# Kernel optimization log

Hardware: AMD Instinct MI355X
Metric: run time of the kernel (lower is better)

The kernel has to match this reference:

```python
import jax, jax.numpy as jnp
import numpy as np
import math

D_MODEL = 1024
N_HEADS = 16
D_K = D_MODEL // N_HEADS
B, S = 4, 1024
MAX_REL = 64  # table built for 2*64-1 positions, clamped beyond


def setup_inputs() -> dict:
    key = jax.random.key(0)
    ks = jax.random.split(key, 11)
    init = 1.0 / math.sqrt(D_MODEL)
    def lin(k):
        kw, kb = jax.random.split(k)
        W = jax.random.uniform(kw, (D_MODEL, D_MODEL), jnp.float32, -init, init)
        b = jax.random.uniform(kb, (D_MODEL,), jnp.float32, -init, init)
        return W, b
    wq, bq = lin(ks[0]); wk, bk = lin(ks[1]); wv, bv = lin(ks[2]); wo, bo = lin(ks[3])
    x = jax.random.normal(ks[4], (B, S, D_MODEL), jnp.float32)
    rel_table = jax.random.normal(ks[5], (2 * MAX_REL - 1, N_HEADS), jnp.float32)
    mask = jnp.ones((B, 1, 1, S), jnp.int32)
    return {"x": x, "mask": mask, "wq": wq, "bq": bq, "wk": wk, "bk": bk,
            "wv": wv, "bv": bv, "wo": wo, "bo": bo, "rel_table": rel_table}


def reference(x, mask, wq, bq, wk, bk, wv, bv, wo, bo, rel_table):
    Bn, Sn, Dm = x.shape
    scale = math.sqrt(D_K)
    def heads(y):  # [B,S,D] -> [B,H,S,dk]
        return y.reshape(Bn, Sn, N_HEADS, D_K).transpose(0, 2, 1, 3)
    Q = heads(x @ wq.T + bq)
    K = heads(x @ wk.T + bk)
    V = heads(x @ wv.T + bv)
    scores = jnp.einsum('bhqd,bhkd->bhqk', Q, K) / scale
    # relative position bias gather, clamped to table range
    rel = jnp.arange(Sn)[None, :] - jnp.arange(Sn)[:, None] + MAX_REL - 1
    rel = jnp.clip(rel, 0, 2 * MAX_REL - 2)
    bias = rel_table[rel]                      # [S,S,H]
    scores = scores + bias.transpose(2, 0, 1)[None]  # [B,H,S,S]
    scores = jnp.where(mask == 0, jnp.float32(-1e9), scores)
    attn = jax.nn.softmax(scores, axis=-1)
    ctx = jnp.einsum('bhqk,bhkd->bhqd', attn, V)
    ctx = ctx.transpose(0, 2, 1, 3).reshape(Bn, Sn, Dm)
    return ctx @ wo.T + bo
```

## Files before the change

### kernel.cpp

```cpp
#include <hip/hip_runtime.h>
#include <hip/hip_bf16.h>

typedef __attribute__((ext_vector_type(8))) short short8;
typedef __attribute__((ext_vector_type(4))) short short4v;
typedef __attribute__((ext_vector_type(4))) float f32x4;

#define D_MODEL 1024
#define N_HEADS 16
#define D_KK 64
#define BATCH 4
#define SEQ 1024
#define NTOK (BATCH*SEQ)

#define LOG2E  1.44269504f
#define SCALE2 (0.125f * 1.44269504f)
#define NEGBIG (-1.44269504e9f)

#if __has_builtin(__builtin_amdgcn_mfma_f32_16x16x16bf16_1k)
#define HAVE_MFMA16 1
#else
#define HAVE_MFMA16 0
#endif

#if __has_builtin(__builtin_amdgcn_exp2f)
#define EXP2(x) __builtin_amdgcn_exp2f(x)
#else
#define EXP2(x) exp2f(x)
#endif

template<int N> struct ic { static constexpr int value = N; };

__device__ __forceinline__ short f2b(float f){
  unsigned u = __float_as_uint(f);
  u += 0x7fffu + ((u >> 16) & 1u);
  return (short)(u >> 16);
}

__device__ __forceinline__ void gl2lds16(const void* g, void* l){
  __builtin_amdgcn_global_load_lds(
      (const __attribute__((address_space(1))) void*)g,
      (__attribute__((address_space(3))) void*)l, 16, 0, 0);
}

__device__ __forceinline__ float max3f(float a, float b, float c){
  float d; asm("v_max3_f32 %0, %1, %2, %3" : "=v"(d) : "v"(a), "v"(b), "v"(c)); return d;
}
__device__ __forceinline__ float tmax16(const f32x4* sc){
  float t = max3f(sc[0][0], sc[0][1], sc[0][2]);
  t = max3f(t, sc[0][3], sc[1][0]);
  t = max3f(t, sc[1][1], sc[1][2]);
  t = max3f(t, sc[1][3], sc[2][0]);
  t = max3f(t, sc[2][1], sc[2][2]);
  t = max3f(t, sc[2][3], sc[3][0]);
  t = max3f(t, sc[3][1], sc[3][2]);
  return fmaxf(t, sc[3][3]);
}

__global__ __launch_bounds__(256) void cvt_all_kernel(
    const float* __restrict__ x,  const float* __restrict__ wq,
    const float* __restrict__ wk, const float* __restrict__ wv,
    const float* __restrict__ wo, short* __restrict__ dst)
{
  const size_t NX = (size_t)NTOK * D_MODEL;
  const size_t NW = (size_t)D_MODEL * D_MODEL;
  size_t e = ((size_t)blockIdx.x * 256 + threadIdx.x) * 4;
  const float* s;
  size_t off;
  if      (e < NX)        { s = x;  off = e; }
  else if (e < NX +   NW) { s = wq; off = e - NX; }
  else if (e < NX + 2*NW) { s = wk; off = e - NX -   NW; }
  else if (e < NX + 3*NW) { s = wv; off = e - NX - 2*NW; }
  else                    { s = wo; off = e - NX - 3*NW; }
  f32x4 v = *reinterpret_cast<const f32x4*>(s + off);
  short4v o;
  o[0]=f2b(v[0]); o[1]=f2b(v[1]); o[2]=f2b(v[2]); o[3]=f2b(v[3]);
  *reinterpret_cast<short4v*>(dst + e) = o;
}

__global__ __launch_bounds__(256) void qkv_gemm_kernel(
    const short* __restrict__ X,
    const short* __restrict__ Wq, const short* __restrict__ Wk, const short* __restrict__ Wv,
    const float* __restrict__ bq, const float* __restrict__ bk, const float* __restrict__ bv,
    short* __restrict__ Q, short* __restrict__ K, short* __restrict__ V)
{
  __shared__ short As[128*64];
  __shared__ short Bs[3][64*64];
  const int bid = blockIdx.x;
  const int xcd = bid & 7, s = bid >> 3;
  const int bn0 = (s >> 2) * 64;
  const int bm0 = (xcd * 4 + (s & 3)) * 128;

  const int tid = threadIdx.x, lane = tid & 63, w = tid >> 6;
  const int wr = w >> 1, wc = w & 1;
  const int srow = lane >> 3;
  const int scol = ((lane & 7) ^ srow) * 8;
  const int fr = lane & 15, g = lane >> 4;

  const short* const Wz[3] = {Wq, Wk, Wv};

  f32x4 acc[3][4][2];
  #pragma unroll
  for (int z=0;z<3;z++)
    #pragma unroll
    for (int m=0;m<4;m++)
      #pragma unroll
      for (int n=0;n<2;n++) acc[z][m][n] = (f32x4){0.f,0.f,0.f,0.f};

  for (int k0 = 0; k0 < D_MODEL; k0 += 64){
    __syncthreads();
    #pragma unroll
    for (int i=0;i<4;i++){
      const int c = w*4 + i;
      gl2lds16(X + (size_t)(bm0 + c*8 + srow)*D_MODEL + k0 + scol, &As[c*8*64]);
    }
    #pragma unroll
    for (int z=0;z<3;z++)
      #pragma unroll
      for (int i=0;i<2;i++){
        const int c = w*2 + i;
        gl2lds16(Wz[z] + (size_t)(bn0 + c*8 + srow)*D_MODEL + k0 + scol, &Bs[z][c*8*64]);
      }
    __syncthreads();
    #pragma unroll
    for (int f=0; f<2; f++){
      short8 af[4];
      #pragma unroll
      for (int m=0;m<4;m++){
        const int rr = wr*64 + m*16 + fr;
        af[m] = *reinterpret_cast<const short8*>(
            (const char*)As + rr*128 + ((g*16 + f*64) ^ ((rr&7)<<4)));
      }
      #pragma unroll
      for (int z=0;z<3;z++){
        short8 bfr[2];
        #pragma unroll
        for (int n=0;n<2;n++){
          const int rr = wc*32 + n*16 + fr;
          bfr[n] = *reinterpret_cast<const short8*>(
              (const char*)&Bs[z][0] + rr*128 + ((g*16 + f*64) ^ ((rr&7)<<4)));
        }
        #pragma unroll
        for (int m=0;m<4;m++)
          #pragma unroll
          for (int n=0;n<2;n++)
            acc[z][m][n] = __builtin_amdgcn_mfma_f32_16x16x32_bf16(af[m], bfr[n], acc[z][m][n], 0,0,0);
      }
    }
  }

  #pragma unroll
  for (int z=0;z<3;z++){
    const float* bias = (z==0) ? bq : (z==1) ? bk : bv;
    #pragma unroll
    for (int n=0;n<2;n++){
      const int col = bn0 + wc*32 + n*16 + fr;
      const float bv_ = bias[col];
      #pragma unroll
      for (int m=0;m<4;m++){
        const int row0 = bm0 + wr*64 + m*16 + g*4;
        if (z == 2){
          const int hh = col >> 6, dd = col & 63;
          const int bb = row0 >> 10, ss = row0 & 1023;
          short4v o;
          #pragma unroll
          for (int r=0;r<4;r++) o[r] = f2b(acc[z][m][n][r] + bv_);
          *reinterpret_cast<short4v*>(
              V + ((size_t)(bb*N_HEADS+hh)*D_KK + dd)*SEQ + ss) = o;
        } else {
          short* O = (z==0) ? Q : K;
          #pragma unroll
          for (int r=0;r<4;r++){
            float v = acc[z][m][n][r] + bv_;
            if (z == 0) v *= SCALE2;
            O[(size_t)(row0+r)*D_MODEL + col] = f2b(v);
          }
        }
      }
    }
  }
}

template<int BN, int MODE, bool PRESC>
__device__ __forceinline__ void gemm_bt_body(const short* __restrict__ A,
    const short* __restrict__ W, const float* __restrict__ bias,
    void* __restrict__ Cout, int N, int K, int bm0, int bn0,
    short* AsB, short* BsB)
{
  constexpr int NF = BN / 32;
  const int tid = threadIdx.x, lane = tid & 63, w = tid >> 6;
  const int wr = w >> 1, wc = w & 1;
  const int srow = lane >> 3;
  const int scol = ((lane & 7) ^ srow) * 8;
  const int fr = lane & 15, g = lane >> 4;

  f32x4 acc[4][NF];
  #pragma unroll
  for (int m=0;m<4;m++)
    #pragma unroll
    for (int n=0;n<NF;n++) acc[m][n] = (f32x4){0.f,0.f,0.f,0.f};

  for (int k0 = 0; k0 < K; k0 += 64){
    __syncthreads();
    #pragma unroll
    for (int i=0;i<4;i++){
      const int c = w*4 + i;
      gl2lds16(A + (size_t)(bm0 + c*8 + srow)*K + k0 + scol, &AsB[c*8*64]);
    }
    #pragma unroll
    for (int i=0;i<NF;i++){
      const int c = w*NF + i;
      gl2lds16(W + (size_t)(bn0 + c*8 + srow)*K + k0 + scol, &BsB[c*8*64]);
    }
    __syncthreads();
    #pragma unroll
    for (int f=0; f<2; f++){
      short8 af[4], bfr[NF];
      #pragma unroll
      for (int m=0;m<4;m++){
        const int rr = wr*64 + m*16 + fr;
        af[m] = *reinterpret_cast<const short8*>(
            (const char*)AsB + rr*128 + ((g*16 + f*64) ^ ((rr&7)<<4)));
      }
      #pragma unroll
      for (int n=0;n<NF;n++){
        const int rr = wc*(BN/2) + n*16 + fr;
        bfr[n] = *reinterpret_cast<const short8*>(
            (const char*)BsB + rr*128 + ((g*16 + f*64) ^ ((rr&7)<<4)));
      }
      #pragma unroll
      for (int m=0;m<4;m++)
        #pragma unroll
        for (int n=0;n<NF;n++)
          acc[m][n] = __builtin_amdgcn_mfma_f32_16x16x32_bf16(af[m], bfr[n], acc[m][n], 0,0,0);
    }
  }

  #pragma unroll
  for (int n=0;n<NF;n++){
    const int col = bn0 + wc*(BN/2) + n*16 + fr;
    const float bv = bias[col];
    #pragma unroll
    for (int m=0;m<4;m++){
      const int row0 = bm0 + wr*64 + m*16 + g*4;
      #pragma unroll
      for (int r=0;r<4;r++){
        float v = acc[m][n][r] + bv;
        if (PRESC) v *= SCALE2;
        if (MODE == 1) ((float*)Cout)[(size_t)(row0+r)*N + col] = v;
        else           ((short*)Cout)[(size_t)(row0+r)*N + col] = f2b(v);
      }
    }
  }
}

__global__ __launch_bounds__(256) void out_gemm_kernel(
    const short* __restrict__ Ctx, const short* __restrict__ Wo,
    const float* __restrict__ bo, float* __restrict__ Out)
{
  __shared__ short As[128*64];
  __shared__ short Bs[64*64];
  const int bid = blockIdx.x;
  const int xcd = bid & 7, s = bid >> 3;
  const int bn0 = (s >> 2) * 64;
  const int bm0 = (xcd * 4 + (s & 3)) * 128;
  gemm_bt_body<64,1,false>(Ctx, Wo, bo, Out, D_MODEL, D_MODEL, bm0, bn0, As, Bs);
}

__global__ __launch_bounds__(512, 2) void attn_kernel(
    const short* __restrict__ Qb, const short* __restrict__ Kb,
    const short* __restrict__ Vtg, const int* __restrict__ mask,
    const float* __restrict__ rel_table, short* __restrict__ Ctx)
{
  const int bid = blockIdx.x;
  const int xcd = bid & 7, slot = bid >> 3;
  const int bh = xcd * 8 + (slot >> 3);
  const int qt = slot & 7;
  const int b = bh >> 4, h = bh & 15;
  const int q0 = qt * 128;
  const int tid = threadIdx.x, lane = tid & 63, w = tid >> 6;
  const int team = w >> 2, wt = w & 3;
  const int fr = lane & 15, g = lane >> 4;

  __shared__ short kvbuf[2][2][2][64][64];
  __shared__ float rel_pad[384];
  __shared__ float mb_all[2][8][64];
  __shared__ float ml[128][2];

  for (int i = tid; i < 384; i += 512){
    int d = i - 128;
    d = d < 0 ? 0 : (d > 126 ? 126 : d);
    rel_pad[i] = rel_table[d * N_HEADS + h] * LOG2E;
  }
  const float cb_lo = rel_table[0*N_HEADS + h]   * LOG2E;
  const float cb_hi = rel_table[126*N_HEADS + h] * LOG2E;

  for (int e = tid; e < 1024; e += 512){
    const int tm = e >> 9, tt = (e >> 6) & 7, i = e & 63;
    const int kvt = tm*512 + tt*64;
    const int delta = kvt - q0;
    const bool far = (delta <= -128 || delta >= 192);
    const float cb = far ? (delta > 0 ? cb_hi : cb_lo) : 0.f;
    mb_all[tm][tt][i] = mask[b*SEQ + kvt + i] ? cb : NEGBIG;
  }

  const short* Qg = Qb + (size_t)b*SEQ*D_MODEL + h*D_KK;
  const short* Kg = Kb + (size_t)b*SEQ*D_MODEL + h*D_KK;
  const short* Vg = Vtg + (size_t)bh*D_KK*SEQ;

  const int qa = q0 + wt*32 + fr;
  const int qb = qa + 16;
  short8 qfa[2], qfb[2];
  #pragma unroll
  for (int f=0; f<2; f++){
    qfa[f] = *reinterpret_cast<const short8*>(Qg + (size_t)qa*D_MODEL + g*8 + f*32);
    qfb[f] = *reinterpret_cast<const short8*>(Qg + (size_t)qb*D_MODEL + g*8 + f*32);
  }

  const char* lds0 = (const char*)kvbuf;
  const int swzb = (fr & 7) << 4;
  const char* kp[2];
  #pragma unroll
  for (int f=0; f<2; f++)
    kp[f] = lds0 + team*16384 + fr*128 + ((g*16 + f*64) ^ swzb);
  const char* vp[4];
  #pragma unroll
  for (int kt=0; kt<4; kt++)
    vp[kt] = lds0 + 32768 + team*16384 + fr*128
           + ((((kt*2 + (g>>1)) ^ (fr&7)) << 4) + (g&1)*8);
  const char* mbp0 = (const char*)mb_all + team*2048 + g*16;

  f32x4 ctxa[4], ctxb[4];
  #pragma unroll
  for (int dt=0; dt<4; dt++){ ctxa[dt] = (f32x4){0.f,0.f,0.f,0.f}; ctxb[dt] = ctxa[dt]; }
  float mruna = -3.0e38f, lruna = 0.f, mrunb = -3.0e38f, lrunb = 0.f;

  const int srow = lane >> 3;
  const int scol = ((lane & 7) ^ srow) * 8;
  auto stage = [&](int buf, int kv0){
    #pragma unroll
    for (int i=0;i<2;i++){
      const int c = wt*2 + i;
      gl2lds16(Kg + (size_t)(kv0 + c*8 + srow)*D_MODEL + scol, &kvbuf[0][team][buf][c*8][0]);
      gl2lds16(Vg + (size_t)(c*8 + srow)*SEQ + kv0 + scol,     &kvbuf[1][team][buf][c*8][0]);
    }
  };

  auto tile_step = [&](auto BUFC, auto VMC, int kv0, int tt) __attribute__((always_inline)) {
    constexpr int BUFL = decltype(BUFC)::value;
    constexpr int VM   = decltype(VMC)::value;

    if constexpr (VM == 4) asm volatile("s_waitcnt vmcnt(4)" ::: "memory");
    else                   asm volatile("s_waitcnt vmcnt(0)" ::: "memory");
    __builtin_amdgcn_s_barrier();
    asm volatile("" ::: "memory");

    const char* mbp = mbp0 + tt*256;

    f32x4 sca[4], scb[4];
    const int delta = kv0 - q0;
    if (delta <= -128 || delta >= 192){
      #pragma unroll
      for (int kt=0;kt<4;kt++){
        f32x4 mb4 = *reinterpret_cast<const f32x4*>(mbp + kt*64);
        sca[kt] = mb4;
        scb[kt] = mb4;
      }
    } else {
      const int pbase = delta + 63 - (wt*32 + fr) + 128 + g*4;
      f32x4 rr[5];
      #pragma unroll
      for (int j=0;j<5;j++)
        #pragma unroll
        for (int r=0;r<4;r++)
          rr[j][r] = rel_pad[pbase - 16 + j*16 + r];
      #pragma unroll
      for (int kt=0;kt<4;kt++){
        f32x4 mb4 = *reinterpret_cast<const f32x4*>(mbp + kt*64);
        #pragma unroll
        for (int r=0;r<4;r++){
          sca[kt][r] = rr[kt+1][r] + mb4[r];
          scb[kt][r] = rr[kt][r]   + mb4[r];
        }
      }
    }

    __builtin_amdgcn_s_setprio(1);
    #pragma unroll
    for (int kt=0;kt<4;kt++){
      #pragma unroll
      for (int f=0;f<2;f++){
        short8 kf = *reinterpret_cast<const short8*>(kp[f] + (kt*2048 + BUFL*8192));
        sca[kt] = __builtin_amdgcn_mfma_f32_16x16x32_bf16(kf, qfa[f], sca[kt], 0,0,0);
        scb[kt] = __builtin_amdgcn_mfma_f32_16x16x32_bf16(kf, qfb[f], scb[kt], 0,0,0);
      }
    }
    __builtin_amdgcn_s_setprio(0);

    short4v paa[4], pab[4];
    {
      const float tmax = tmax16(sca);
      if (!__all(tmax <= mruna + 8.f)){
        float tm = fmaxf(tmax, __shfl_xor(tmax, 16));
        tm = fmaxf(tm, __shfl_xor(tm, 32));
        const float mnew = fmaxf(mruna, tm);
        const float corr = EXP2(mruna - mnew);
        lruna *= corr;
        #pragma unroll
        for (int dt=0;dt<4;dt++)
          #pragma unroll
          for (int r=0;r<4;r++) ctxa[dt][r] *= corr;
        mruna = mnew;
      }
      float psum = 0.f;
      #pragma unroll
      for (int kt=0;kt<4;kt++){
        float p0 = EXP2(sca[kt][0] - mruna);
        float p1 = EXP2(sca[kt][1] - mruna);
        float p2 = EXP2(sca[kt][2] - mruna);
        float p3 = EXP2(sca[kt][3] - mruna);
        psum += (p0 + p1) + (p2 + p3);
        union { short4v s; __hip_bfloat162 hh[2]; } u;
        u.hh[0] = __float22bfloat162_rn(make_float2(p0, p1));
        u.hh[1] = __float22bfloat162_rn(make_float2(p2, p3));
        paa[kt] = u.s;
      }
      lruna += psum;
    }
    {
      const float tmax = tmax16(scb);
      if (!__all(tmax <= mrunb + 8.f)){
        float tm = fmaxf(tmax, __shfl_xor(tmax, 16));
        tm = fmaxf(tm, __shfl_xor(tm, 32));
        const float mnew = fmaxf(mrunb, tm);
        const float corr = EXP2(mrunb - mnew);
        lrunb *= corr;
        #pragma unroll
        for (int dt=0;dt<4;dt++)
          #pragma unroll
          for (int r=0;r<4;r++) ctxb[dt][r] *= corr;
        mrunb = mnew;
      }
      float psum = 0.f;
      #pragma unroll
      for (int kt=0;kt<4;kt++){
        float p0 = EXP2(scb[kt][0] - mrunb);
        float p1 = EXP2(scb[kt][1] - mrunb);
        float p2 = EXP2(scb[kt][2] - mrunb);
        float p3 = EXP2(scb[kt][3] - mrunb);
        psum += (p0 + p1) + (p2 + p3);
        union { short4v s; __hip_bfloat162 hh[2]; } u;
        u.hh[0] = __float22bfloat162_rn(make_float2(p0, p1));
        u.hh[1] = __float22bfloat162_rn(make_float2(p2, p3));
        pab[kt] = u.s;
      }
      lrunb += psum;
    }

    __builtin_amdgcn_s_setprio(1);
#if HAVE_MFMA16
    #pragma unroll
    for (int dt=0;dt<4;dt++){
      #pragma unroll
      for (int kt=0;kt<4;kt++){
        short4v va = *reinterpret_cast<const short4v*>(vp[kt] + (dt*2048 + BUFL*8192));
        ctxa[dt] = __builtin_amdgcn_mfma_f32_16x16x16bf16_1k(va, paa[kt], ctxa[dt], 0,0,0);
        ctxb[dt] = __builtin_amdgcn_mfma_f32_16x16x16bf16_1k(va, pab[kt], ctxb[dt], 0,0,0);
      }
    }
#else
    const char* vsb = lds0 + 32768 + team*16384 + BUFL*8192;
    #pragma unroll
    for (int f=0;f<2;f++){
      union { short8 s8; unsigned u[4]; } bfa, bfb;
      #pragma unroll
      for (int m=0;m<4;m++){
        const int srcl = ((g&1)*2 + (m>>1))*16 + fr;
        union { short4v s; unsigned u[2]; } ca0, ca1, cb0, cb1;
        ca0.s = paa[f*2+0]; ca1.s = paa[f*2+1];
        cb0.s = pab[f*2+0]; cb1.s = pab[f*2+1];
        unsigned a0 = __shfl((int)ca0.u[m&1], srcl);
        unsigned a1 = __shfl((int)ca1.u[m&1], srcl);
        bfa.u[m] = (g >> 1) ? a1 : a0;
        unsigned b0 = __shfl((int)cb0.u[m&1], srcl);
        unsigned b1 = __shfl((int)cb1.u[m&1], srcl);
        bfb.u[m] = (g >> 1) ? b1 : b0;
      }
      #pragma unroll
      for (int dt=0;dt<4;dt++){
        const int dr = dt*16 + fr;
        const int vswz = (dr & 7) << 4;
        short8 va = *reinterpret_cast<const short8*>(
            vsb + dr*128 + ((g*16 + f*64) ^ vswz));
        ctxa[dt] = __builtin_amdgcn_mfma_f32_16x16x32_bf16(va, bfa.s8, ctxa[dt], 0,0,0);
        ctxb[dt] = __builtin_amdgcn_mfma_f32_16x16x32_bf16(va, bfb.s8, ctxb[dt], 0,0,0);
      }
    }
#endif
    __builtin_amdgcn_s_setprio(0);

    asm volatile("" ::: "memory");
    __builtin_amdgcn_s_barrier();
  };

  const int kvbase = team * 512;
  __syncthreads();
  stage(0, kvbase);
  stage(1, kvbase + 64);

  for (int t = 0; t < 6; t += 2){
    tile_step(ic<0>{}, ic<4>{}, kvbase + t*64,     t);
    stage(0, kvbase + (t+2)*64);
    tile_step(ic<1>{}, ic<4>{}, kvbase + (t+1)*64, t+1);
    stage(1, kvbase + (t+3)*64);
  }
  tile_step(ic<0>{}, ic<4>{}, kvbase + 6*64, 6);
  tile_step(ic<1>{}, ic<0>{}, kvbase + 7*64, 7);
  asm volatile("" ::: "memory");

  lruna += __shfl_xor(lruna, 16);
  lruna += __shfl_xor(lruna, 32);
  lrunb += __shfl_xor(lrunb, 16);
  lrunb += __shfl_xor(lrunb, 32);

  float* mctx = (float*)&kvbuf[0][0][0][0][0];
  const int rowA = wt*32 + fr, rowB = rowA + 16;
  if (team == 1){
    #pragma unroll
    for (int dt=0;dt<4;dt++){
      *reinterpret_cast<f32x4*>(&mctx[rowA*72 + dt*16 + g*4]) = ctxa[dt];
      *reinterpret_cast<f32x4*>(&mctx[rowB*72 + dt*16 + g*4]) = ctxb[dt];
    }
    ml[rowA][0] = mruna; ml[rowA][1] = lruna;
    ml[rowB][0] = mrunb; ml[rowB][1] = lrunb;
  }
  __syncthreads();
  if (team == 0){
    {
      const float m1 = ml[rowA][0], l1 = ml[rowA][1];
      const float m  = fmaxf(mruna, m1);
      const float s0 = EXP2(mruna - m), s1 = EXP2(m1 - m);
      const float rl = 1.f / (lruna*s0 + l1*s1);
      #pragma unroll
      for (int dt=0;dt<4;dt++){
        f32x4 c1 = *reinterpret_cast<const f32x4*>(&mctx[rowA*72 + dt*16 + g*4]);
        short4v o;
        #pragma unroll
        for (int r=0;r<4;r++) o[r] = f2b((ctxa[dt][r]*s0 + c1[r]*s1) * rl);
        *reinterpret_cast<short4v*>(
            Ctx + (size_t)(b*SEQ + qa)*D_MODEL + h*D_KK + dt*16 + g*4) = o;
      }
    }
    {
      const float m1 = ml[rowB][0], l1 = ml[rowB][1];
      const float m  = fmaxf(mrunb, m1);
      const float s0 = EXP2(mrunb - m), s1 = EXP2(m1 - m);
      const float rl = 1.f / (lrunb*s0 + l1*s1);
      #pragma unroll
      for (int dt=0;dt<4;dt++){
        f32x4 c1 = *reinterpret_cast<const f32x4*>(&mctx[rowB*72 + dt*16 + g*4]);
        short4v o;
        #pragma unroll
        for (int r=0;r<4;r++) o[r] = f2b((ctxb[dt][r]*s0 + c1[r]*s1) * rl);
        *reinterpret_cast<short4v*>(
            Ctx + (size_t)(b*SEQ + qb)*D_MODEL + h*D_KK + dt*16 + g*4) = o;
      }
    }
  }
}

extern "C" void kernel_launch(void* const* d_in, const int* in_sizes, int n_in,
                              void* d_out, int out_size, void* d_ws, size_t ws_size,
                              hipStream_t stream) {
  const float* x    = (const float*)d_in[0];
  const int*   mask = (const int*)  d_in[1];
  const float* wq   = (const float*)d_in[2];
  const float* bq   = (const float*)d_in[3];
  const float* wk   = (const float*)d_in[4];
  const float* bk   = (const float*)d_in[5];
  const float* wv   = (const float*)d_in[6];
  const float* bv   = (const float*)d_in[7];
  const float* wo   = (const float*)d_in[8];
  const float* bo   = (const float*)d_in[9];
  const float* rel  = (const float*)d_in[10];

  const size_t NX = (size_t)NTOK * D_MODEL;
  const size_t NW = (size_t)D_MODEL * D_MODEL;
  if (ws_size < (NX + 4*NW + 4*NX) * sizeof(short)) return;
  short* xb   = (short*)d_ws;
  short* wqb  = xb  + NX;
  short* wkb  = wqb + NW;
  short* wvb  = wkb + NW;
  short* wob  = wvb + NW;
  short* Qb   = wob + NW;
  short* Kb   = Qb  + NX;
  short* Vtg  = Kb  + NX;
  short* Ctxb = Vtg + NX;

  cvt_all_kernel<<<8192, 256, 0, stream>>>(x, wq, wk, wv, wo, xb);

  qkv_gemm_kernel<<<512, 256, 0, stream>>>(
      xb, wqb, wkb, wvb, bq, bk, bv, Qb, Kb, Vtg);

  attn_kernel<<<512, 512, 0, stream>>>(Qb, Kb, Vtg, mask, rel, Ctxb);

  out_gemm_kernel<<<512, 256, 0, stream>>>(Ctxb, wob, bo, (float*)d_out);
}
```

Measured before the change: 100.3 us.

## Double-buffer LDS tiles in QKV GEMM with vmcnt-based async prefetch

```diff
diff --git a/kernel.cpp b/kernel.cpp
--- a/kernel.cpp
+++ b/kernel.cpp
@@ -83,8 +83,8 @@
     const float* __restrict__ bq, const float* __restrict__ bk, const float* __restrict__ bv,
     short* __restrict__ Q, short* __restrict__ K, short* __restrict__ V)
 {
-  __shared__ short As[128*64];
-  __shared__ short Bs[3][64*64];
+  __shared__ short As[2][128*64];
+  __shared__ short Bs[2][3][64*64];
   const int bid = blockIdx.x;
   const int xcd = bid & 7, s = bid >> 3;
   const int bn0 = (s >> 2) * 64;
@@ -106,21 +106,29 @@
       #pragma unroll
       for (int n=0;n<2;n++) acc[z][m][n] = (f32x4){0.f,0.f,0.f,0.f};
 
-  for (int k0 = 0; k0 < D_MODEL; k0 += 64){
-    __syncthreads();
+  auto stage = [&](int buf, int t){
+    const int k0 = t * 64;
     #pragma unroll
     for (int i=0;i<4;i++){
       const int c = w*4 + i;
-      gl2lds16(X + (size_t)(bm0 + c*8 + srow)*D_MODEL + k0 + scol, &As[c*8*64]);
+      gl2lds16(X + (size_t)(bm0 + c*8 + srow)*D_MODEL + k0 + scol, &As[buf][c*8*64]);
     }
     #pragma unroll
     for (int z=0;z<3;z++)
       #pragma unroll
       for (int i=0;i<2;i++){
         const int c = w*2 + i;
-        gl2lds16(Wz[z] + (size_t)(bn0 + c*8 + srow)*D_MODEL + k0 + scol, &Bs[z][c*8*64]);
-      }
-    __syncthreads();
+        gl2lds16(Wz[z] + (size_t)(bn0 + c*8 + srow)*D_MODEL + k0 + scol, &Bs[buf][z][c*8*64]);
+      }
+  };
+
+  auto kstep = [&](auto BUFC, auto VMC) __attribute__((always_inline)) {
+    constexpr int BUFL = decltype(BUFC)::value;
+    constexpr int VM   = decltype(VMC)::value;
+    if constexpr (VM == 10) asm volatile("s_waitcnt vmcnt(10)" ::: "memory");
+    else                    asm volatile("s_waitcnt vmcnt(0)"  ::: "memory");
+    __builtin_amdgcn_s_barrier();
+    asm volatile("" ::: "memory");
     #pragma unroll
     for (int f=0; f<2; f++){
       short8 af[4];
@@ -128,7 +136,7 @@
       for (int m=0;m<4;m++){
         const int rr = wr*64 + m*16 + fr;
         af[m] = *reinterpret_cast<const short8*>(
-            (const char*)As + rr*128 + ((g*16 + f*64) ^ ((rr&7)<<4)));
+            (const char*)&As[BUFL][0] + rr*128 + ((g*16 + f*64) ^ ((rr&7)<<4)));
       }
       #pragma unroll
       for (int z=0;z<3;z++){
@@ -137,7 +145,7 @@
         for (int n=0;n<2;n++){
           const int rr = wc*32 + n*16 + fr;
           bfr[n] = *reinterpret_cast<const short8*>(
-              (const char*)&Bs[z][0] + rr*128 + ((g*16 + f*64) ^ ((rr&7)<<4)));
+              (const char*)&Bs[BUFL][z][0] + rr*128 + ((g*16 + f*64) ^ ((rr&7)<<4)));
         }
         #pragma unroll
         for (int m=0;m<4;m++)
@@ -146,7 +154,20 @@
             acc[z][m][n] = __builtin_amdgcn_mfma_f32_16x16x32_bf16(af[m], bfr[n], acc[z][m][n], 0,0,0);
       }
     }
-  }
+    asm volatile("" ::: "memory");
+    __builtin_amdgcn_s_barrier();
+  };
+
+  stage(0, 0);
+  stage(1, 1);
+  for (int t = 0; t < 14; t += 2){
+    kstep(ic<0>{}, ic<10>{});
+    stage(0, t+2);
+    kstep(ic<1>{}, ic<10>{});
+    stage(1, t+3);
+  }
+  kstep(ic<0>{}, ic<10>{});
+  kstep(ic<1>{}, ic<0>{});
 
   #pragma unroll
   for (int z=0;z<3;z++){
```

Result: slower. 110.5 us (+10.1%).
